# Kernel optimization log

Hardware: AMD Instinct MI355X
Metric: run time of the kernel (lower is better)

The kernel has to match this reference:

```python
import jax, jax.numpy as jnp
import numpy as np

B, N, M, C = 8, 262144, 100, 7
BOX_WEIGHT = 2.0
EPS = 1e-7


def setup_inputs() -> dict:
    key = jax.random.key(0)
    k0, k1, k2, k3, k4, k5 = jax.random.split(key, 6)
    pred_cls = jax.random.normal(k0, (B, N, C), jnp.float32)
    pred_reg = jax.random.normal(k1, (B, N, 4), jnp.float32)
    anchors = jax.random.uniform(k2, (N, 2), jnp.float32) * 1024.0
    strides = jnp.ones((N,), jnp.float32) * 8.0
    ctr = jax.random.uniform(k3, (B, M, 2), jnp.float32) * 960.0 + 32.0
    wh = jax.random.uniform(k4, (B, M, 2), jnp.float32) * 120.0 + 8.0
    gt_boxes = jnp.concatenate([ctr - wh / 2, ctr + wh / 2], axis=-1)
    gt_labels = jax.random.randint(k5, (B, M), 1, C + 1)  # labels in [1, C]
    return {"pred_cls": pred_cls, "pred_reg": pred_reg, "anchors": anchors,
            "strides": strides, "gt_boxes": gt_boxes, "gt_labels": gt_labels}


def giou_loss(p, g):
    # p, g: (M,4) xyxy; elementwise GIoU loss = 1 - GIoU (torchvision semantics)
    ap = (p[:, 2] - p[:, 0]) * (p[:, 3] - p[:, 1])
    ag = (g[:, 2] - g[:, 0]) * (g[:, 3] - g[:, 1])
    lt = jnp.maximum(p[:, :2], g[:, :2])
    rb = jnp.minimum(p[:, 2:], g[:, 2:])
    whi = jnp.clip(rb - lt, 0.0)
    inter = whi[:, 0] * whi[:, 1]
    union = ap + ag - inter
    iou = inter / (union + EPS)
    ltc = jnp.minimum(p[:, :2], g[:, :2])
    rbc = jnp.maximum(p[:, 2:], g[:, 2:])
    whc = jnp.clip(rbc - ltc, 0.0)
    ac = whc[:, 0] * whc[:, 1]
    giou = iou - (ac - union) / (ac + EPS)
    return 1.0 - giou


def reference(pred_cls, pred_reg, anchors, strides, gt_boxes, gt_labels):
    num_anchors = anchors.shape[0]
    # head.decode_boxes: center+offset, exp size decode (guaranteed valid xyxy)
    s = strides[None, :, None]
    ctr = anchors[None] + pred_reg[..., :2] * s
    wh = jnp.exp(pred_reg[..., 2:]) * s
    pred_boxes = jnp.concatenate([ctr - wh / 2, ctr + wh / 2], axis=-1)  # (B,N,4)

    def per_image(cls_b, boxes_b, gt_b, lab_b):
        # nearest-anchor assignment via cdist (expanded as gemm to avoid (M,N,2))
        gc = (gt_b[:, :2] + gt_b[:, 2:]) / 2.0  # (M,2)
        d2 = (jnp.sum(gc * gc, -1)[:, None] + jnp.sum(anchors * anchors, -1)[None, :]
              - 2.0 * gc @ anchors.T)
        dist = jnp.sqrt(jnp.clip(d2, 0.0))  # (M,N)
        assigned = jnp.argmin(dist, axis=1)  # (M,)
        pos_mask = jnp.zeros((num_anchors,), bool).at[assigned].set(True)
        neg_mask = jnp.min(dist, axis=0) > 3.0
        # scatter one-hot class targets (collisions all set 1.0, order-free)
        cls_id = jnp.clip(lab_b - 1, 0, C - 1)
        tgt = jnp.zeros_like(cls_b).at[assigned, cls_id].set(1.0)
        # BCEWithLogits(mean) then scalar * sample_weight then .mean()  (faithful)
        bce_mean = jnp.mean(jnp.logaddexp(0.0, cls_b) - cls_b * tgt)
        sw = jnp.where(pos_mask, 2.0, 1.0) * jnp.where(neg_mask, 1.0, 0.1)
        loss_cls = bce_mean * jnp.mean(sw)
        # box loss: if #unique assigned anchors == M, original pairs boolean-masked
        # (anchor-index-sorted) preds with gt order; else gathers by assigned_idx
        lb_eq = jnp.mean(giou_loss(boxes_b[jnp.sort(assigned)], gt_b))
        lb_ne = jnp.mean(giou_loss(boxes_b[assigned], gt_b))
        loss_box = jnp.where(jnp.sum(pos_mask) == gt_b.shape[0], lb_eq, lb_ne)
        return loss_cls, loss_box

    lc, lb = jax.vmap(per_image)(pred_cls, pred_boxes, gt_boxes, gt_labels)
    total_cls = jnp.mean(lc)
    total_box = jnp.mean(lb)
    return total_cls + BOX_WEIGHT * total_box
```

## Files before the change

### kernel.cpp

```cpp
#include <hip/hip_runtime.h>

#define B_ 8
#define N_ 262144
#define M_ 100
#define C_ 7
#define EPSF 1e-7f
#define AB_ 2048
#define CH_ (N_ / AB_)
#define APT_ 8
#define SEG_ 4
#define SEGN_ (N_ / SEG_)

typedef unsigned long long ull;

__device__ __forceinline__ float softplus0(float x) {
  return fmaxf(x, 0.0f) + log1pf(expf(-fabsf(x)));
}

__device__ __forceinline__ ull u64min(ull a, ull b) { return b < a ? b : a; }

__global__ void __launch_bounds__(256)
k_main(const float* __restrict__ pred_cls,
       const float* __restrict__ anchors,
       const float* __restrict__ gt_boxes,
       double* __restrict__ sp_sum,
       double* __restrict__ swb_sum,
       ull* __restrict__ part) {
  const int b = blockIdx.y;
  const int c = blockIdx.x;
  const int t = threadIdx.x;

  __shared__ float4 gt4[M_];
  __shared__ float red[256];
  __shared__ ull wb[M_][4];

  if (t < M_) {
    float4 g = reinterpret_cast<const float4*>(gt_boxes)[b * M_ + t];
    float gx = __fmul_rn(__fadd_rn(g.x, g.z), 0.5f);
    float gy = __fmul_rn(__fadd_rn(g.y, g.w), 0.5f);
    gt4[t] = make_float4(gx, gy, __fadd_rn(__fmul_rn(gx, gx), __fmul_rn(gy, gy)), 0.f);
  }

  const float4* pc = reinterpret_cast<const float4*>(
      pred_cls + (size_t)b * (size_t)(N_ * C_) + (size_t)c * (AB_ * C_));
  float acc_sp = 0.f;
  for (int k = 0; k < 14; ++k) {
    float4 v = pc[t + k * 256];
    acc_sp += softplus0(v.x) + softplus0(v.y) + softplus0(v.z) + softplus0(v.w);
  }
  red[t] = acc_sp;
  __syncthreads();
  for (int s = 128; s > 0; s >>= 1) {
    if (t < s) red[t] += red[t + s];
    __syncthreads();
  }
  if (t == 0) atomicAdd(&sp_sum[b], (double)red[0]);

  const int n0 = c * AB_;
  float ax[APT_], ay[APT_], t2[APT_], mind[APT_];
  unsigned nn[APT_];
#pragma unroll
  for (int k = 0; k < APT_; ++k) {
    float2 a = reinterpret_cast<const float2*>(anchors)[n0 + t + k * 256];
    ax[k] = a.x; ay[k] = a.y;
    t2[k] = __fadd_rn(__fmul_rn(a.x, a.x), __fmul_rn(a.y, a.y));
    mind[k] = __int_as_float(0x7f800000);
    nn[k] = (unsigned)(n0 + t + (k << 8));
  }
  const int wid  = t >> 6;
  const int lane = t & 63;
  int bidx[6];
#pragma unroll
  for (int i = 0; i < 6; ++i) bidx[i] = ((lane ^ (1 << i)) << 2);
  __syncthreads();

#pragma unroll 2
  for (int m = 0; m < M_; ++m) {
    const float4 g = gt4[m];
    ull pk = 0xffffffffffffffffULL;
#pragma unroll
    for (int k = 0; k < APT_; ++k) {
      float dot = __fmaf_rn(g.y, ay[k], __fmul_rn(g.x, ax[k]));
      float d2  = __fsub_rn(__fadd_rn(g.z, t2[k]), __fadd_rn(dot, dot));
      d2 = fmaxf(d2, 0.0f);
      mind[k] = fminf(mind[k], d2);
      ull cand = ((ull)__float_as_uint(d2) << 32) | (ull)nn[k];
      pk = u64min(pk, cand);
    }
#pragma unroll
    for (int i = 0; i < 6; ++i) {
      int lo = __builtin_amdgcn_ds_bpermute(bidx[i], (int)(unsigned)(pk & 0xffffffffULL));
      int hi = __builtin_amdgcn_ds_bpermute(bidx[i], (int)(unsigned)(pk >> 32));
      ull o = ((ull)(unsigned)hi << 32) | (ull)(unsigned)lo;
      pk = u64min(pk, o);
    }
    if (lane == 0) wb[m][wid] = pk;
  }
  __syncthreads();

  float accw = 0.f;
#pragma unroll
  for (int k = 0; k < APT_; ++k) accw += (sqrtf(mind[k]) > 3.0f) ? 1.0f : 0.1f;
  red[t] = accw;
  __syncthreads();
  for (int s = 128; s > 0; s >>= 1) {
    if (t < s) red[t] += red[t + s];
    __syncthreads();
  }
  if (t == 0) atomicAdd(&swb_sum[b], (double)red[0]);

  if (t < M_) {
    ull v = u64min(u64min(wb[t][0], wb[t][1]), u64min(wb[t][2], wb[t][3]));
    part[((size_t)(b * M_ + t)) * CH_ + c] = v;
  }
}

__global__ void __launch_bounds__(128)
k_final2(const float* __restrict__ pred_cls,
         const float* __restrict__ pred_reg,
         const float* __restrict__ anchors,
         const float* __restrict__ strides,
         const float* __restrict__ gt_boxes,
         const int* __restrict__ gt_labels,
         const ull* __restrict__ part,
         const double* __restrict__ sp_sum,
         const double* __restrict__ swb_sum,
         float* __restrict__ lc, float* __restrict__ lb) {
  const int b = blockIdx.x;
  const int t = threadIdx.x;
  __shared__ unsigned asg[M_];
  __shared__ int cid[M_];
  __shared__ unsigned srt[M_];
  __shared__ float4 gt4[M_];
  __shared__ float red[128];
  __shared__ int dupCount;
  if (t == 0) dupCount = 0;
  if (t < M_) {
    const ull* p = part + ((size_t)(b * M_ + t)) * CH_;
    ull v0 = 0xffffffffffffffffULL, v1 = v0, v2 = v0, v3 = v0;
    for (int c = 0; c < CH_; c += 4) {
      v0 = u64min(v0, p[c]);
      v1 = u64min(v1, p[c + 1]);
      v2 = u64min(v2, p[c + 2]);
      v3 = u64min(v3, p[c + 3]);
    }
    asg[t] = (unsigned)(u64min(u64min(v0, v1), u64min(v2, v3)) & 0xffffffffULL);
    int cc = gt_labels[b * M_ + t] - 1;
    cc = cc < 0 ? 0 : (cc > C_ - 1 ? C_ - 1 : cc);
    cid[t] = cc;
    float4 g = reinterpret_cast<const float4*>(gt_boxes)[b * M_ + t];
    float gx = __fmul_rn(__fadd_rn(g.x, g.z), 0.5f);
    float gy = __fmul_rn(__fadd_rn(g.y, g.w), 0.5f);
    gt4[t] = make_float4(gx, gy, __fadd_rn(__fmul_rn(gx, gx), __fmul_rn(gy, gy)), 0.f);
  }
  __syncthreads();

  float tg = 0.f, corr = 0.f;
  if (t < M_) {
    bool dupPair = false, dupIdx = false;
    for (int m = 0; m < t; ++m) {
      if (asg[m] == asg[t]) {
        dupIdx = true;
        if (cid[m] == cid[t]) dupPair = true;
      }
    }
    if (!dupPair) tg = pred_cls[((size_t)b * N_ + asg[t]) * C_ + cid[t]];
    if (dupIdx) atomicAdd(&dupCount, 1);
    if (!dupIdx) {
      float2 a = reinterpret_cast<const float2*>(anchors)[asg[t]];
      float t2 = __fadd_rn(__fmul_rn(a.x, a.x), __fmul_rn(a.y, a.y));
      float mind = __int_as_float(0x7f800000);
      for (int m = 0; m < M_; ++m) {
        float4 g = gt4[m];
        float dot = __fmaf_rn(g.y, a.y, __fmul_rn(g.x, a.x));
        float d2  = __fsub_rn(__fadd_rn(g.z, t2), __fadd_rn(dot, dot));
        mind = fminf(mind, fmaxf(d2, 0.0f));
      }
      corr = (sqrtf(mind) > 3.0f) ? 1.0f : 0.1f;
    }
  }
  red[t] = tg;
  __syncthreads();
  for (int s = 64; s > 0; s >>= 1) {
    if (t < s) red[t] += red[t + s];
    __syncthreads();
  }
  const float tgt_total = red[0];
  __syncthreads();
  red[t] = corr;
  __syncthreads();
  for (int s = 64; s > 0; s >>= 1) {
    if (t < s) red[t] += red[t + s];
    __syncthreads();
  }
  const float corr_total = red[0];
  const bool uniqueAll = (dupCount == 0);
  __syncthreads();

  if (uniqueAll && t < M_) {
    const unsigned v = asg[t];
    int rank = 0;
    for (int m = 0; m < M_; ++m) rank += (asg[m] < v) ? 1 : 0;
    srt[rank] = v;
  }
  __syncthreads();

  float gl = 0.f;
  if (t < M_) {
    const unsigned q = uniqueAll ? srt[t] : asg[t];
    float4 r = reinterpret_cast<const float4*>(pred_reg)[(size_t)b * N_ + q];
    float2 a = reinterpret_cast<const float2*>(anchors)[q];
    float s = strides[q];
    float cx = a.x + r.x * s, cy = a.y + r.y * s;
    float hx = (expf(r.z) * s) * 0.5f, hy = (expf(r.w) * s) * 0.5f;
    float px0 = cx - hx, py0 = cy - hy, px1 = cx + hx, py1 = cy + hy;
    float4 g = reinterpret_cast<const float4*>(gt_boxes)[b * M_ + t];
    float ap = (px1 - px0) * (py1 - py0);
    float ag = (g.z - g.x) * (g.w - g.y);
    float ltx = fmaxf(px0, g.x), lty = fmaxf(py0, g.y);
    float rbx = fminf(px1, g.z), rby = fminf(py1, g.w);
    float wix = fmaxf(rbx - ltx, 0.f), wiy = fmaxf(rby - lty, 0.f);
    float inter = wix * wiy;
    float uni = ap + ag - inter;
    float iou = inter / (uni + EPSF);
    float lcx = fminf(px0, g.x), lcy = fminf(py0, g.y);
    float rcx = fmaxf(px1, g.z), rcy = fmaxf(py1, g.w);
    float wcx = fmaxf(rcx - lcx, 0.f), wcy = fmaxf(rcy - lcy, 0.f);
    float ac = wcx * wcy;
    float giou = iou - (ac - uni) / (ac + EPSF);
    gl = 1.f - giou;
  }
  __syncthreads();
  red[t] = gl;
  __syncthreads();
  for (int s = 64; s > 0; s >>= 1) {
    if (t < s) red[t] += red[t + s];
    __syncthreads();
  }
  if (t == 0) {
    lb[b] = red[0] / (float)M_;
    float bce = (float)((sp_sum[b] - (double)tgt_total) / (double)(N_ * C_));
    float swm = (float)((swb_sum[b] + (double)corr_total) / (double)N_);
    lc[b] = bce * swm;
  }
}

__global__ void __launch_bounds__(256)
k_passA(const float* __restrict__ pred_cls,
        const float* __restrict__ anchors,
        const float* __restrict__ gt_boxes,
        double* __restrict__ sp_sum,
        double* __restrict__ swb_sum) {
  const int b = blockIdx.y;
  const int c = blockIdx.x;
  const int t = threadIdx.x;
  __shared__ float4 gt4[M_];
  __shared__ float red[256];
  if (t < M_) {
    float4 g = reinterpret_cast<const float4*>(gt_boxes)[b * M_ + t];
    float gx = __fmul_rn(__fadd_rn(g.x, g.z), 0.5f);
    float gy = __fmul_rn(__fadd_rn(g.y, g.w), 0.5f);
    gt4[t] = make_float4(gx, gy, __fadd_rn(__fmul_rn(gx, gx), __fmul_rn(gy, gy)), 0.f);
  }
  const float4* pc = reinterpret_cast<const float4*>(
      pred_cls + (size_t)b * (size_t)(N_ * C_) + (size_t)c * (1024 * C_));
  float acc_sp = 0.f;
#pragma unroll
  for (int k = 0; k < 7; ++k) {
    float4 v = pc[t + k * 256];
    acc_sp += softplus0(v.x) + softplus0(v.y) + softplus0(v.z) + softplus0(v.w);
  }
  red[t] = acc_sp;
  __syncthreads();
  for (int s = 128; s > 0; s >>= 1) {
    if (t < s) red[t] += red[t + s];
    __syncthreads();
  }
  if (t == 0) atomicAdd(&sp_sum[b], (double)red[0]);
  const int n0 = c * 1024;
  float ax[4], ay[4], t2[4], mind[4];
#pragma unroll
  for (int k = 0; k < 4; ++k) {
    float2 a = reinterpret_cast<const float2*>(anchors)[n0 + t + k * 256];
    ax[k] = a.x; ay[k] = a.y;
    t2[k] = __fadd_rn(__fmul_rn(a.x, a.x), __fmul_rn(a.y, a.y));
    mind[k] = __int_as_float(0x7f800000);
  }
#pragma unroll 2
  for (int m = 0; m < M_; ++m) {
    const float4 g = gt4[m];
#pragma unroll
    for (int k = 0; k < 4; ++k) {
      float dot = __fmaf_rn(g.y, ay[k], __fmul_rn(g.x, ax[k]));
      float d2  = __fsub_rn(__fadd_rn(g.z, t2[k]), __fadd_rn(dot, dot));
      mind[k] = fminf(mind[k], fmaxf(d2, 0.0f));
    }
  }
  float accw = 0.f;
#pragma unroll
  for (int k = 0; k < 4; ++k) accw += (sqrtf(mind[k]) > 3.0f) ? 1.0f : 0.1f;
  __syncthreads();
  red[t] = accw;
  __syncthreads();
  for (int s = 128; s > 0; s >>= 1) {
    if (t < s) red[t] += red[t + s];
    __syncthreads();
  }
  if (t == 0) atomicAdd(&swb_sum[b], (double)red[0]);
}

__global__ void __launch_bounds__(256)
k_argmin(const float* __restrict__ anchors,
         const float* __restrict__ gt_boxes,
         ull* __restrict__ amin) {
  const int bm  = blockIdx.y;
  const int seg = blockIdx.x;
  const float4 g = reinterpret_cast<const float4*>(gt_boxes)[bm];
  const float gx = __fmul_rn(__fadd_rn(g.x, g.z), 0.5f);
  const float gy = __fmul_rn(__fadd_rn(g.y, g.w), 0.5f);
  const float t1 = __fadd_rn(__fmul_rn(gx, gx), __fmul_rn(gy, gy));
  const float2* an = reinterpret_cast<const float2*>(anchors);
  float best = __int_as_float(0x7f800000);
  unsigned bestn = 0;
  const int n0 = seg * SEGN_;
#pragma unroll 4
  for (int n = n0 + threadIdx.x; n < n0 + SEGN_; n += 256) {
    float2 a = an[n];
    float t2  = __fadd_rn(__fmul_rn(a.x, a.x), __fmul_rn(a.y, a.y));
    float dot = __fmaf_rn(gy, a.y, __fmul_rn(gx, a.x));
    float d2  = __fsub_rn(__fadd_rn(t1, t2), __fadd_rn(dot, dot));
    d2 = fmaxf(d2, 0.0f);
    if (d2 < best) { best = d2; bestn = (unsigned)n; }
  }
  ull pk = ((ull)__float_as_uint(best) << 32) | (ull)bestn;
  __shared__ ull red[256];
  const int t = threadIdx.x;
  red[t] = pk;
  __syncthreads();
  for (int s = 128; s > 0; s >>= 1) {
    if (t < s) {
      ull o = red[t + s];
      if (o < red[t]) red[t] = o;
    }
    __syncthreads();
  }
  if (t == 0) atomicMin(&amin[bm], red[0]);
}

__global__ void __launch_bounds__(128)
k_final_img(const float* __restrict__ pred_cls,
            const float* __restrict__ pred_reg,
            const float* __restrict__ anchors,
            const float* __restrict__ strides,
            const float* __restrict__ gt_boxes,
            const int* __restrict__ gt_labels,
            const ull* __restrict__ amin,
            const double* __restrict__ sp_sum,
            const double* __restrict__ swb_sum,
            float* __restrict__ lc, float* __restrict__ lb) {
  const int b = blockIdx.x;
  const int t = threadIdx.x;
  __shared__ unsigned asg[M_];
  __shared__ int cid[M_];
  __shared__ unsigned srt[M_];
  __shared__ float4 gt4[M_];
  __shared__ float red[128];
  __shared__ int dupCount;
  if (t == 0) dupCount = 0;
  if (t < M_) {
    asg[t] = (unsigned)(amin[b * M_ + t] & 0xffffffffULL);
    int c = gt_labels[b * M_ + t] - 1;
    c = c < 0 ? 0 : (c > C_ - 1 ? C_ - 1 : c);
    cid[t] = c;
    float4 g = reinterpret_cast<const float4*>(gt_boxes)[b * M_ + t];
    float gx = __fmul_rn(__fadd_rn(g.x, g.z), 0.5f);
    float gy = __fmul_rn(__fadd_rn(g.y, g.w), 0.5f);
    gt4[t] = make_float4(gx, gy, __fadd_rn(__fmul_rn(gx, gx), __fmul_rn(gy, gy)), 0.f);
  }
  __syncthreads();

  float tg = 0.f, corr = 0.f;
  if (t < M_) {
    bool dupPair = false, dupIdx = false;
    for (int m = 0; m < t; ++m) {
      if (asg[m] == asg[t]) {
        dupIdx = true;
        if (cid[m] == cid[t]) dupPair = true;
      }
    }
    if (!dupPair) tg = pred_cls[((size_t)b * N_ + asg[t]) * C_ + cid[t]];
    if (dupIdx) atomicAdd(&dupCount, 1);
    if (!dupIdx) {
      float2 a = reinterpret_cast<const float2*>(anchors)[asg[t]];
      float t2 = __fadd_rn(__fmul_rn(a.x, a.x), __fmul_rn(a.y, a.y));
      float mind = __int_as_float(0x7f800000);
      for (int m = 0; m < M_; ++m) {
        float4 g = gt4[m];
        float dot = __fmaf_rn(g.y, a.y, __fmul_rn(g.x, a.x));
        float d2  = __fsub_rn(__fadd_rn(g.z, t2), __fadd_rn(dot, dot));
        mind = fminf(mind, fmaxf(d2, 0.0f));
      }
      corr = (sqrtf(mind) > 3.0f) ? 1.0f : 0.1f;
    }
  }
  red[t] = tg;
  __syncthreads();
  for (int s = 64; s > 0; s >>= 1) {
    if (t < s) red[t] += red[t + s];
    __syncthreads();
  }
  const float tgt_total = red[0];
  __syncthreads();
  red[t] = corr;
  __syncthreads();
  for (int s = 64; s > 0; s >>= 1) {
    if (t < s) red[t] += red[t + s];
    __syncthreads();
  }
  const float corr_total = red[0];
  const bool uniqueAll = (dupCount == 0);
  __syncthreads();

  if (uniqueAll && t < M_) {
    const unsigned v = asg[t];
    int rank = 0;
    for (int m = 0; m < M_; ++m) rank += (asg[m] < v) ? 1 : 0;
    srt[rank] = v;
  }
  __syncthreads();

  float gl = 0.f;
  if (t < M_) {
    const unsigned q = uniqueAll ? srt[t] : asg[t];
    float4 r = reinterpret_cast<const float4*>(pred_reg)[(size_t)b * N_ + q];
    float2 a = reinterpret_cast<const float2*>(anchors)[q];
    float s = strides[q];
    float cx = a.x + r.x * s, cy = a.y + r.y * s;
    float hx = (expf(r.z) * s) * 0.5f, hy = (expf(r.w) * s) * 0.5f;
    float px0 = cx - hx, py0 = cy - hy, px1 = cx + hx, py1 = cy + hy;
    float4 g = reinterpret_cast<const float4*>(gt_boxes)[b * M_ + t];
    float ap = (px1 - px0) * (py1 - py0);
    float ag = (g.z - g.x) * (g.w - g.y);
    float ltx = fmaxf(px0, g.x), lty = fmaxf(py0, g.y);
    float rbx = fminf(px1, g.z), rby = fminf(py1, g.w);
    float wix = fmaxf(rbx - ltx, 0.f), wiy = fmaxf(rby - lty, 0.f);
    float inter = wix * wiy;
    float uni = ap + ag - inter;
    float iou = inter / (uni + EPSF);
    float lcx = fminf(px0, g.x), lcy = fminf(py0, g.y);
    float rcx = fmaxf(px1, g.z), rcy = fmaxf(py1, g.w);
    float wcx = fmaxf(rcx - lcx, 0.f), wcy = fmaxf(rcy - lcy, 0.f);
    float ac = wcx * wcy;
    float giou = iou - (ac - uni) / (ac + EPSF);
    gl = 1.f - giou;
  }
  __syncthreads();
  red[t] = gl;
  __syncthreads();
  for (int s = 64; s > 0; s >>= 1) {
    if (t < s) red[t] += red[t + s];
    __syncthreads();
  }
  if (t == 0) {
    lb[b] = red[0] / (float)M_;
    float bce = (float)((sp_sum[b] - (double)tgt_total) / (double)(N_ * C_));
    float swm = (float)((swb_sum[b] + (double)corr_total) / (double)N_);
    lc[b] = bce * swm;
  }
}

__global__ void __launch_bounds__(64)
k_total(const float* __restrict__ lc, const float* __restrict__ lb,
        float* __restrict__ out) {
  if (threadIdx.x == 0 && blockIdx.x == 0) {
    float sc = 0.f, sb = 0.f;
    for (int b = 0; b < B_; ++b) { sc += lc[b]; sb += lb[b]; }
    out[0] = sc / 8.0f + 2.0f * (sb / 8.0f);
  }
}

extern "C" void kernel_launch(void* const* d_in, const int* in_sizes, int n_in,
                              void* d_out, int out_size, void* d_ws, size_t ws_size,
                              hipStream_t stream) {
  (void)in_sizes; (void)n_in; (void)out_size;
  const float* pred_cls  = (const float*)d_in[0];
  const float* pred_reg  = (const float*)d_in[1];
  const float* anchors   = (const float*)d_in[2];
  const float* strides   = (const float*)d_in[3];
  const float* gt_boxes  = (const float*)d_in[4];
  const int*   gt_labels = (const int*)d_in[5];
  float* out = (float*)d_out;

  char* ws = (char*)d_ws;
  double* sp_sum  = (double*)(ws);
  double* swb_sum = (double*)(ws + 64);

  const size_t part_off = 128;
  const size_t part_bytes = (size_t)B_ * M_ * CH_ * 8;
  const size_t tail_off = part_off + part_bytes;
  const size_t need = tail_off + 64 + 64;

  if (ws_size >= need) {
    ull* part = (ull*)(ws + part_off);
    float* lc = (float*)(ws + tail_off);
    float* lb = (float*)(ws + tail_off + 64);

    hipMemsetAsync(ws, 0, 128, stream);
    k_main<<<dim3(CH_, B_), dim3(256), 0, stream>>>(pred_cls, anchors, gt_boxes,
                                                    sp_sum, swb_sum, part);
    k_final2<<<dim3(B_), dim3(128), 0, stream>>>(pred_cls, pred_reg, anchors,
                                                 strides, gt_boxes, gt_labels,
                                                 part, sp_sum, swb_sum, lc, lb);
    k_total<<<dim3(1), dim3(64), 0, stream>>>(lc, lb, out);
  } else {
    ull* amin = (ull*)(ws + 128);
    float* lc = (float*)(ws + 128 + 6400);
    float* lb = (float*)(ws + 128 + 6400 + 32);
    hipMemsetAsync(ws, 0, 128, stream);
    hipMemsetAsync(ws + 128, 0xFF, 6400, stream);
    k_passA<<<dim3(N_ / 1024, B_), dim3(256), 0, stream>>>(pred_cls, anchors, gt_boxes,
                                                           sp_sum, swb_sum);
    k_argmin<<<dim3(SEG_, B_ * M_), dim3(256), 0, stream>>>(anchors, gt_boxes, amin);
    k_final_img<<<dim3(B_), dim3(128), 0, stream>>>(pred_cls, pred_reg, anchors,
                                                    strides, gt_boxes, gt_labels,
                                                    amin, sp_sum, swb_sum, lc, lb);
    k_total<<<dim3(1), dim3(64), 0, stream>>>(lc, lb, out);
  }
}
```

Baseline: 249.5 us.

## Pack distance math, shorten shuffle tree, fuse final kernels into one launch

Anchor distance computation now uses 2-wide float vectors so packed FMA/min/max can be used. Each thread first picks its best local anchor with scalar compares and only a 3-step cross-lane shuffle runs per gt box, with the remaining reduction done through shared memory. Double atomics are replaced by per-block partial sums, which drops the memset. The per-image final kernel and the total kernel are merged into a single 1024-thread block. The aims are less ALU and shuffle work in the hot loop and fewer launches, at the cost of a larger shared-memory reduction and a serial tail in one block.

Result: slower. 261.0 us (+4.6%).

```diff
diff --git a/kernel.cpp b/kernel.cpp
--- a/kernel.cpp
+++ b/kernel.cpp
@@ -7,11 +7,11 @@
 #define EPSF 1e-7f
 #define AB_ 2048
 #define CH_ (N_ / AB_)
-#define APT_ 8
 #define SEG_ 4
 #define SEGN_ (N_ / SEG_)
 
 typedef unsigned long long ull;
+typedef float v2f __attribute__((ext_vector_type(2)));
 
 __device__ __forceinline__ float softplus0(float x) {
   return fmaxf(x, 0.0f) + log1pf(expf(-fabsf(x)));
@@ -23,8 +23,8 @@
 k_main(const float* __restrict__ pred_cls,
        const float* __restrict__ anchors,
        const float* __restrict__ gt_boxes,
-       double* __restrict__ sp_sum,
-       double* __restrict__ swb_sum,
+       float* __restrict__ sp_part,
+       float* __restrict__ sw_part,
        ull* __restrict__ part) {
   const int b = blockIdx.y;
   const int c = blockIdx.x;
@@ -32,7 +32,7 @@
 
   __shared__ float4 gt4[M_];
   __shared__ float red[256];
-  __shared__ ull wb[M_][4];
+  __shared__ ull wb[M_][33];
 
   if (t < M_) {
     float4 g = reinterpret_cast<const float4*>(gt_boxes)[b * M_ + t];
@@ -54,124 +54,164 @@
     if (t < s) red[t] += red[t + s];
     __syncthreads();
   }
-  if (t == 0) atomicAdd(&sp_sum[b], (double)red[0]);
+  if (t == 0) sp_part[b * CH_ + c] = red[0];
 
   const int n0 = c * AB_;
-  float ax[APT_], ay[APT_], t2[APT_], mind[APT_];
-  unsigned nn[APT_];
-#pragma unroll
-  for (int k = 0; k < APT_; ++k) {
-    float2 a = reinterpret_cast<const float2*>(anchors)[n0 + t + k * 256];
-    ax[k] = a.x; ay[k] = a.y;
-    t2[k] = __fadd_rn(__fmul_rn(a.x, a.x), __fmul_rn(a.y, a.y));
-    mind[k] = __int_as_float(0x7f800000);
-    nn[k] = (unsigned)(n0 + t + (k << 8));
-  }
-  const int wid  = t >> 6;
+  const float2* an = reinterpret_cast<const float2*>(anchors);
+  v2f ax2[4], ay2[4], t22[4], mind2[4];
+#pragma unroll
+  for (int q = 0; q < 4; ++q) {
+    float2 a0 = an[n0 + t + (2 * q) * 256];
+    float2 a1 = an[n0 + t + (2 * q + 1) * 256];
+    ax2[q] = (v2f){a0.x, a1.x};
+    ay2[q] = (v2f){a0.y, a1.y};
+    t22[q] = (v2f){__fadd_rn(__fmul_rn(a0.x, a0.x), __fmul_rn(a0.y, a0.y)),
+                   __fadd_rn(__fmul_rn(a1.x, a1.x), __fmul_rn(a1.y, a1.y))};
+    mind2[q] = (v2f){__int_as_float(0x7f800000), __int_as_float(0x7f800000)};
+  }
   const int lane = t & 63;
-  int bidx[6];
-#pragma unroll
-  for (int i = 0; i < 6; ++i) bidx[i] = ((lane ^ (1 << i)) << 2);
-  __syncthreads();
-
+  int bidx[3];
+#pragma unroll
+  for (int i = 0; i < 3; ++i) bidx[i] = ((lane ^ (1 << i)) << 2);
+  __syncthreads();
+
+  const v2f zero2 = (v2f){0.f, 0.f};
 #pragma unroll 2
   for (int m = 0; m < M_; ++m) {
     const float4 g = gt4[m];
-    ull pk = 0xffffffffffffffffULL;
-#pragma unroll
-    for (int k = 0; k < APT_; ++k) {
-      float dot = __fmaf_rn(g.y, ay[k], __fmul_rn(g.x, ax[k]));
-      float d2  = __fsub_rn(__fadd_rn(g.z, t2[k]), __fadd_rn(dot, dot));
-      d2 = fmaxf(d2, 0.0f);
-      mind[k] = fminf(mind[k], d2);
-      ull cand = ((ull)__float_as_uint(d2) << 32) | (ull)nn[k];
-      pk = u64min(pk, cand);
-    }
-#pragma unroll
-    for (int i = 0; i < 6; ++i) {
+    const v2f gx2 = (v2f){g.x, g.x};
+    const v2f gy2 = (v2f){g.y, g.y};
+    const v2f gz2 = (v2f){g.z, g.z};
+    float bd = __int_as_float(0x7f800000);
+    int bk = 0;
+#pragma unroll
+    for (int q = 0; q < 4; ++q) {
+      v2f gmul = gx2 * ax2[q];
+      v2f dot  = __builtin_elementwise_fma(gy2, ay2[q], gmul);
+      v2f d2   = (gz2 + t22[q]) - (dot + dot);
+      d2 = __builtin_elementwise_max(d2, zero2);
+      mind2[q] = __builtin_elementwise_min(mind2[q], d2);
+      if (d2.x < bd) { bd = d2.x; bk = 2 * q; }
+      if (d2.y < bd) { bd = d2.y; bk = 2 * q + 1; }
+    }
+    ull pk = ((ull)__float_as_uint(bd) << 32) |
+             (ull)(unsigned)(n0 + t + (bk << 8));
+#pragma unroll
+    for (int i = 0; i < 3; ++i) {
       int lo = __builtin_amdgcn_ds_bpermute(bidx[i], (int)(unsigned)(pk & 0xffffffffULL));
       int hi = __builtin_amdgcn_ds_bpermute(bidx[i], (int)(unsigned)(pk >> 32));
       ull o = ((ull)(unsigned)hi << 32) | (ull)(unsigned)lo;
       pk = u64min(pk, o);
     }
-    if (lane == 0) wb[m][wid] = pk;
+    if ((t & 7) == 0) wb[m][t >> 3] = pk;
   }
   __syncthreads();
 
   float accw = 0.f;
 #pragma unroll
-  for (int k = 0; k < APT_; ++k) accw += (sqrtf(mind[k]) > 3.0f) ? 1.0f : 0.1f;
+  for (int q = 0; q < 4; ++q) {
+    accw += (sqrtf(mind2[q].x) > 3.0f) ? 1.0f : 0.1f;
+    accw += (sqrtf(mind2[q].y) > 3.0f) ? 1.0f : 0.1f;
+  }
   red[t] = accw;
   __syncthreads();
   for (int s = 128; s > 0; s >>= 1) {
     if (t < s) red[t] += red[t + s];
     __syncthreads();
   }
-  if (t == 0) atomicAdd(&swb_sum[b], (double)red[0]);
+  if (t == 0) sw_part[b * CH_ + c] = red[0];
 
   if (t < M_) {
-    ull v = u64min(u64min(wb[t][0], wb[t][1]), u64min(wb[t][2], wb[t][3]));
-    part[((size_t)(b * M_ + t)) * CH_ + c] = v;
-  }
-}
-
-__global__ void __launch_bounds__(128)
-k_final2(const float* __restrict__ pred_cls,
-         const float* __restrict__ pred_reg,
-         const float* __restrict__ anchors,
-         const float* __restrict__ strides,
-         const float* __restrict__ gt_boxes,
-         const int* __restrict__ gt_labels,
-         const ull* __restrict__ part,
-         const double* __restrict__ sp_sum,
-         const double* __restrict__ swb_sum,
-         float* __restrict__ lc, float* __restrict__ lb) {
-  const int b = blockIdx.x;
-  const int t = threadIdx.x;
-  __shared__ unsigned asg[M_];
-  __shared__ int cid[M_];
-  __shared__ unsigned srt[M_];
-  __shared__ float4 gt4[M_];
-  __shared__ float red[128];
-  __shared__ int dupCount;
-  if (t == 0) dupCount = 0;
-  if (t < M_) {
-    const ull* p = part + ((size_t)(b * M_ + t)) * CH_;
-    ull v0 = 0xffffffffffffffffULL, v1 = v0, v2 = v0, v3 = v0;
-    for (int c = 0; c < CH_; c += 4) {
+    const ull* w = wb[t];
+    ull v0 = w[0], v1 = w[1], v2 = w[2], v3 = w[3];
+    for (int j = 4; j < 32; j += 4) {
+      v0 = u64min(v0, w[j]);
+      v1 = u64min(v1, w[j + 1]);
+      v2 = u64min(v2, w[j + 2]);
+      v3 = u64min(v3, w[j + 3]);
+    }
+    part[((size_t)(b * M_ + t)) * CH_ + c] = u64min(u64min(v0, v1), u64min(v2, v3));
+  }
+}
+
+__global__ void __launch_bounds__(1024)
+k_finalall(const float* __restrict__ pred_cls,
+           const float* __restrict__ pred_reg,
+           const float* __restrict__ anchors,
+           const float* __restrict__ strides,
+           const float* __restrict__ gt_boxes,
+           const int* __restrict__ gt_labels,
+           const ull* __restrict__ part,
+           const float* __restrict__ sp_part,
+           const float* __restrict__ sw_part,
+           float* __restrict__ out) {
+  const int t  = threadIdx.x;
+  const int b  = t >> 7;
+  const int tt = t & 127;
+  __shared__ float4 gt4[B_][M_];
+  __shared__ unsigned asg[B_][M_];
+  __shared__ int cid[B_][M_];
+  __shared__ unsigned srt[B_][M_];
+  __shared__ float red[B_][128];
+  __shared__ double redd[B_][128];
+  __shared__ int dup[B_];
+  __shared__ float tgtT[B_], corrT[B_], lcs[B_], lbs[B_];
+  __shared__ double spT[B_], swT[B_];
+
+  if (tt == 0) dup[b] = 0;
+  if (tt < M_) {
+    const ull* p = part + ((size_t)(b * M_ + tt)) * CH_;
+    ull v0 = p[0], v1 = p[1], v2 = p[2], v3 = p[3];
+    for (int c = 4; c < CH_; c += 4) {
       v0 = u64min(v0, p[c]);
       v1 = u64min(v1, p[c + 1]);
       v2 = u64min(v2, p[c + 2]);
       v3 = u64min(v3, p[c + 3]);
     }
-    asg[t] = (unsigned)(u64min(u64min(v0, v1), u64min(v2, v3)) & 0xffffffffULL);
-    int cc = gt_labels[b * M_ + t] - 1;
+    asg[b][tt] = (unsigned)(u64min(u64min(v0, v1), u64min(v2, v3)) & 0xffffffffULL);
+    int cc = gt_labels[b * M_ + tt] - 1;
     cc = cc < 0 ? 0 : (cc > C_ - 1 ? C_ - 1 : cc);
-    cid[t] = cc;
-    float4 g = reinterpret_cast<const float4*>(gt_boxes)[b * M_ + t];
+    cid[b][tt] = cc;
+    float4 g = reinterpret_cast<const float4*>(gt_boxes)[b * M_ + tt];
     float gx = __fmul_rn(__fadd_rn(g.x, g.z), 0.5f);
     float gy = __fmul_rn(__fadd_rn(g.y, g.w), 0.5f);
-    gt4[t] = make_float4(gx, gy, __fadd_rn(__fmul_rn(gx, gx), __fmul_rn(gy, gy)), 0.f);
-  }
+    gt4[b][tt] = make_float4(gx, gy, __fadd_rn(__fmul_rn(gx, gx), __fmul_rn(gy, gy)), 0.f);
+  }
+
+  redd[b][tt] = (double)sp_part[b * CH_ + tt];
+  __syncthreads();
+  for (int s = 64; s > 0; s >>= 1) {
+    if (tt < s) redd[b][tt] += redd[b][tt + s];
+    __syncthreads();
+  }
+  if (tt == 0) spT[b] = redd[b][0];
+  __syncthreads();
+  redd[b][tt] = (double)sw_part[b * CH_ + tt];
+  __syncthreads();
+  for (int s = 64; s > 0; s >>= 1) {
+    if (tt < s) redd[b][tt] += redd[b][tt + s];
+    __syncthreads();
+  }
+  if (tt == 0) swT[b] = redd[b][0];
   __syncthreads();
 
   float tg = 0.f, corr = 0.f;
-  if (t < M_) {
+  if (tt < M_) {
     bool dupPair = false, dupIdx = false;
-    for (int m = 0; m < t; ++m) {
-      if (asg[m] == asg[t]) {
+    for (int m = 0; m < tt; ++m) {
+      if (asg[b][m] == asg[b][tt]) {
         dupIdx = true;
-        if (cid[m] == cid[t]) dupPair = true;
+        if (cid[b][m] == cid[b][tt]) dupPair = true;
       }
     }
-    if (!dupPair) tg = pred_cls[((size_t)b * N_ + asg[t]) * C_ + cid[t]];
-    if (dupIdx) atomicAdd(&dupCount, 1);
+    if (!dupPair) tg = pred_cls[((size_t)b * N_ + asg[b][tt]) * C_ + cid[b][tt]];
+    if (dupIdx) atomicAdd(&dup[b], 1);
     if (!dupIdx) {
-      float2 a = reinterpret_cast<const float2*>(anchors)[asg[t]];
+      float2 a = reinterpret_cast<const float2*>(anchors)[asg[b][tt]];
       float t2 = __fadd_rn(__fmul_rn(a.x, a.x), __fmul_rn(a.y, a.y));
       float mind = __int_as_float(0x7f800000);
       for (int m = 0; m < M_; ++m) {
-        float4 g = gt4[m];
+        float4 g = gt4[b][m];
         float dot = __fmaf_rn(g.y, a.y, __fmul_rn(g.x, a.x));
         float d2  = __fsub_rn(__fadd_rn(g.z, t2), __fadd_rn(dot, dot));
         mind = fminf(mind, fmaxf(d2, 0.0f));
@@ -179,42 +219,42 @@
       corr = (sqrtf(mind) > 3.0f) ? 1.0f : 0.1f;
     }
   }
-  red[t] = tg;
-  __syncthreads();
-  for (int s = 64; s > 0; s >>= 1) {
-    if (t < s) red[t] += red[t + s];
-    __syncthreads();
-  }
-  const float tgt_total = red[0];
-  __syncthreads();
-  red[t] = corr;
-  __syncthreads();
-  for (int s = 64; s > 0; s >>= 1) {
-    if (t < s) red[t] += red[t + s];
-    __syncthreads();
-  }
-  const float corr_total = red[0];
-  const bool uniqueAll = (dupCount == 0);
-  __syncthreads();
-
-  if (uniqueAll && t < M_) {
-    const unsigned v = asg[t];
+  red[b][tt] = tg;
+  __syncthreads();
+  for (int s = 64; s > 0; s >>= 1) {
+    if (tt < s) red[b][tt] += red[b][tt + s];
+    __syncthreads();
+  }
+  if (tt == 0) tgtT[b] = red[b][0];
+  __syncthreads();
+  red[b][tt] = corr;
+  __syncthreads();
+  for (int s = 64; s > 0; s >>= 1) {
+    if (tt < s) red[b][tt] += red[b][tt + s];
+    __syncthreads();
+  }
+  if (tt == 0) corrT[b] = red[b][0];
+  __syncthreads();
+  const bool uniqueAll = (dup[b] == 0);
+
+  if (uniqueAll && tt < M_) {
+    const unsigned v = asg[b][tt];
     int rank = 0;
-    for (int m = 0; m < M_; ++m) rank += (asg[m] < v) ? 1 : 0;
-    srt[rank] = v;
+    for (int m = 0; m < M_; ++m) rank += (asg[b][m] < v) ? 1 : 0;
+    srt[b][rank] = v;
   }
   __syncthreads();
 
   float gl = 0.f;
-  if (t < M_) {
-    const unsigned q = uniqueAll ? srt[t] : asg[t];
+  if (tt < M_) {
+    const unsigned q = uniqueAll ? srt[b][tt] : asg[b][tt];
     float4 r = reinterpret_cast<const float4*>(pred_reg)[(size_t)b * N_ + q];
     float2 a = reinterpret_cast<const float2*>(anchors)[q];
     float s = strides[q];
     float cx = a.x + r.x * s, cy = a.y + r.y * s;
     float hx = (expf(r.z) * s) * 0.5f, hy = (expf(r.w) * s) * 0.5f;
     float px0 = cx - hx, py0 = cy - hy, px1 = cx + hx, py1 = cy + hy;
-    float4 g = reinterpret_cast<const float4*>(gt_boxes)[b * M_ + t];
+    float4 g = reinterpret_cast<const float4*>(gt_boxes)[b * M_ + tt];
     float ap = (px1 - px0) * (py1 - py0);
     float ag = (g.z - g.x) * (g.w - g.y);
     float ltx = fmaxf(px0, g.x), lty = fmaxf(py0, g.y);
@@ -231,17 +271,23 @@
     gl = 1.f - giou;
   }
   __syncthreads();
-  red[t] = gl;
-  __syncthreads();
-  for (int s = 64; s > 0; s >>= 1) {
-    if (t < s) red[t] += red[t + s];
-    __syncthreads();
-  }
+  red[b][tt] = gl;
+  __syncthreads();
+  for (int s = 64; s > 0; s >>= 1) {
+    if (tt < s) red[b][tt] += red[b][tt + s];
+    __syncthreads();
+  }
+  if (tt == 0) {
+    lbs[b] = red[b][0] / (float)M_;
+    float bce = (float)((spT[b] - (double)tgtT[b]) / (double)(N_ * C_));
+    float swm = (float)((swT[b] + (double)corrT[b]) / (double)N_);
+    lcs[b] = bce * swm;
+  }
+  __syncthreads();
   if (t == 0) {
-    lb[b] = red[0] / (float)M_;
-    float bce = (float)((sp_sum[b] - (double)tgt_total) / (double)(N_ * C_));
-    float swm = (float)((swb_sum[b] + (double)corr_total) / (double)N_);
-    lc[b] = bce * swm;
+    float sc = 0.f, sb = 0.f;
+    for (int i = 0; i < B_; ++i) { sc += lcs[i]; sb += lbs[i]; }
+    out[0] = sc / 8.0f + 2.0f * (sb / 8.0f);
   }
 }
 
@@ -492,27 +538,23 @@
   float* out = (float*)d_out;
 
   char* ws = (char*)d_ws;
-  double* sp_sum  = (double*)(ws);
-  double* swb_sum = (double*)(ws + 64);
-
-  const size_t part_off = 128;
   const size_t part_bytes = (size_t)B_ * M_ * CH_ * 8;
-  const size_t tail_off = part_off + part_bytes;
-  const size_t need = tail_off + 64 + 64;
+  const size_t sp_off = part_bytes;
+  const size_t sw_off = sp_off + 4096;
+  const size_t need   = sw_off + 4096;
 
   if (ws_size >= need) {
-    ull* part = (ull*)(ws + part_off);
-    float* lc = (float*)(ws + tail_off);
-    float* lb = (float*)(ws + tail_off + 64);
-
-    hipMemsetAsync(ws, 0, 128, stream);
+    ull*   part    = (ull*)ws;
+    float* sp_part = (float*)(ws + sp_off);
+    float* sw_part = (float*)(ws + sw_off);
     k_main<<<dim3(CH_, B_), dim3(256), 0, stream>>>(pred_cls, anchors, gt_boxes,
-                                                    sp_sum, swb_sum, part);
-    k_final2<<<dim3(B_), dim3(128), 0, stream>>>(pred_cls, pred_reg, anchors,
-                                                 strides, gt_boxes, gt_labels,
-                                                 part, sp_sum, swb_sum, lc, lb);
-    k_total<<<dim3(1), dim3(64), 0, stream>>>(lc, lb, out);
+                                                    sp_part, sw_part, part);
+    k_finalall<<<dim3(1), dim3(1024), 0, stream>>>(pred_cls, pred_reg, anchors,
+                                                   strides, gt_boxes, gt_labels,
+                                                   part, sp_part, sw_part, out);
   } else {
+    double* sp_sum  = (double*)(ws);
+    double* swb_sum = (double*)(ws + 64);
     ull* amin = (ull*)(ws + 128);
     float* lc = (float*)(ws + 128 + 6400);
     float* lb = (float*)(ws + 128 + 6400 + 32);
```

## Replace brute-force anchor distance scan with uniform-grid spatial hashing

Applied to the files above, without the earlier changes.

Builds a 64x64 uniform grid over the anchors (count, scan, scatter) and uses it to find each GT's nearest anchor through expanding ring search. The same grid marks anchors within radius 3 of any GT in a byte map, which replaces the full M×N min-distance pass. This removes the O(B·M·N) distance computation that dominated k_main. In exchange it adds several small kernels, scattered gathers through the grid and a memset of a B·N byte map, and it relies on the ring termination bound being conservative enough to give exact ties.

Result: faster. 225.6 us (-9.6%).

```diff
diff --git a/kernel.cpp b/kernel.cpp
--- a/kernel.cpp
+++ b/kernel.cpp
@@ -7,11 +7,15 @@
 #define EPSF 1e-7f
 #define AB_ 2048
 #define CH_ (N_ / AB_)
-#define APT_ 8
+#define GXC 64
+#define CELLW 16.0f
+#define INV_CELL 0.0625f
+#define NCELL (GXC * GXC)
 #define SEG_ 4
 #define SEGN_ (N_ / SEG_)
 
 typedef unsigned long long ull;
+typedef unsigned int u32;
 
 __device__ __forceinline__ float softplus0(float x) {
   return fmaxf(x, 0.0f) + log1pf(expf(-fabsf(x)));
@@ -19,28 +23,135 @@
 
 __device__ __forceinline__ ull u64min(ull a, ull b) { return b < a ? b : a; }
 
+__device__ __forceinline__ int cell_of(float2 a) {
+  int ix = (int)(a.x * INV_CELL); ix = ix < 0 ? 0 : (ix > GXC - 1 ? GXC - 1 : ix);
+  int iy = (int)(a.y * INV_CELL); iy = iy < 0 ? 0 : (iy > GXC - 1 ? GXC - 1 : iy);
+  return iy * GXC + ix;
+}
+
+__device__ __forceinline__ float d2_exact(float gx, float gy, float t1, float2 a) {
+  float t2  = __fadd_rn(__fmul_rn(a.x, a.x), __fmul_rn(a.y, a.y));
+  float dot = __fmaf_rn(gy, a.y, __fmul_rn(gx, a.x));
+  return __fsub_rn(__fadd_rn(t1, t2), __fadd_rn(dot, dot));
+}
+
 __global__ void __launch_bounds__(256)
-k_main(const float* __restrict__ pred_cls,
-       const float* __restrict__ anchors,
-       const float* __restrict__ gt_boxes,
-       double* __restrict__ sp_sum,
-       double* __restrict__ swb_sum,
-       ull* __restrict__ part) {
-  const int b = blockIdx.y;
-  const int c = blockIdx.x;
+k_count(const float* __restrict__ anchors, u32* __restrict__ hist) {
+  const int n = blockIdx.x * 256 + threadIdx.x;
+  float2 a = reinterpret_cast<const float2*>(anchors)[n];
+  atomicAdd(&hist[cell_of(a)], 1u);
+}
+
+__global__ void __launch_bounds__(1024)
+k_scan(u32* __restrict__ hist ,
+       u32* __restrict__ cellStart) {
+  __shared__ u32 sA[1024];
   const int t = threadIdx.x;
-
-  __shared__ float4 gt4[M_];
+  u32 h0 = hist[4 * t], h1 = hist[4 * t + 1], h2 = hist[4 * t + 2], h3 = hist[4 * t + 3];
+  u32 s = h0 + h1 + h2 + h3;
+  sA[t] = s;
+  __syncthreads();
+  for (int off = 1; off < 1024; off <<= 1) {
+    u32 add = (t >= off) ? sA[t - off] : 0u;
+    __syncthreads();
+    sA[t] += add;
+    __syncthreads();
+  }
+  u32 excl = sA[t] - s;
+  u32 e0 = excl, e1 = e0 + h0, e2 = e1 + h1, e3 = e2 + h2;
+  cellStart[4 * t] = e0; cellStart[4 * t + 1] = e1;
+  cellStart[4 * t + 2] = e2; cellStart[4 * t + 3] = e3;
+  hist[4 * t] = e0; hist[4 * t + 1] = e1;
+  hist[4 * t + 2] = e2; hist[4 * t + 3] = e3;
+  if (t == 1023) cellStart[NCELL] = sA[1023];
+}
+
+__global__ void __launch_bounds__(256)
+k_scatter(const float* __restrict__ anchors, u32* __restrict__ cur,
+          u32* __restrict__ aidx) {
+  const int n = blockIdx.x * 256 + threadIdx.x;
+  float2 a = reinterpret_cast<const float2*>(anchors)[n];
+  u32 pos = atomicAdd(&cur[cell_of(a)], 1u);
+  aidx[pos] = (u32)n;
+}
+
+__global__ void __launch_bounds__(64)
+k_assign(const float* __restrict__ anchors,
+         const float* __restrict__ gt_boxes,
+         const u32* __restrict__ cellStart,
+         const u32* __restrict__ aidx,
+         unsigned char* __restrict__ map,
+         ull* __restrict__ amin) {
+  const int m = blockIdx.x, b = blockIdx.y;
+  const int lane = threadIdx.x;
+  const float4 g = reinterpret_cast<const float4*>(gt_boxes)[b * M_ + m];
+  const float gx = __fmul_rn(__fadd_rn(g.x, g.z), 0.5f);
+  const float gy = __fmul_rn(__fadd_rn(g.y, g.w), 0.5f);
+  const float t1 = __fadd_rn(__fmul_rn(gx, gx), __fmul_rn(gy, gy));
+  const float2* an = reinterpret_cast<const float2*>(anchors);
+  unsigned char* mp = map + (size_t)b * N_;
+
+  {
+    int x0 = (int)floorf((gx - 3.5f) * INV_CELL); x0 = x0 < 0 ? 0 : (x0 > GXC - 1 ? GXC - 1 : x0);
+    int x1 = (int)floorf((gx + 3.5f) * INV_CELL); x1 = x1 < 0 ? 0 : (x1 > GXC - 1 ? GXC - 1 : x1);
+    int y0 = (int)floorf((gy - 3.5f) * INV_CELL); y0 = y0 < 0 ? 0 : (y0 > GXC - 1 ? GXC - 1 : y0);
+    int y1 = (int)floorf((gy + 3.5f) * INV_CELL); y1 = y1 < 0 ? 0 : (y1 > GXC - 1 ? GXC - 1 : y1);
+    for (int cy = y0; cy <= y1; ++cy)
+      for (int cx = x0; cx <= x1; ++cx) {
+        u32 s = cellStart[cy * GXC + cx], e = cellStart[cy * GXC + cx + 1];
+        for (u32 j = s + lane; j < e; j += 64) {
+          u32 n = aidx[j];
+          if (d2_exact(gx, gy, t1, an[n]) <= 9.0f) mp[n] = 1;
+        }
+      }
+  }
+
+  int cx0 = (int)(gx * INV_CELL); cx0 = cx0 < 0 ? 0 : (cx0 > GXC - 1 ? GXC - 1 : cx0);
+  int cy0 = (int)(gy * INV_CELL); cy0 = cy0 < 0 ? 0 : (cy0 > GXC - 1 ? GXC - 1 : cy0);
+  int bidx[6];
+#pragma unroll
+  for (int i = 0; i < 6; ++i) bidx[i] = ((lane ^ (1 << i)) << 2);
+
+  ull best = 0xffffffffffffffffULL;
+  for (int ring = 1; ring < GXC; ++ring) {
+    best = 0xffffffffffffffffULL;
+    int x0 = cx0 - ring < 0 ? 0 : cx0 - ring;
+    int x1 = cx0 + ring > GXC - 1 ? GXC - 1 : cx0 + ring;
+    int y0 = cy0 - ring < 0 ? 0 : cy0 - ring;
+    int y1 = cy0 + ring > GXC - 1 ? GXC - 1 : cy0 + ring;
+    for (int cy = y0; cy <= y1; ++cy)
+      for (int cx = x0; cx <= x1; ++cx) {
+        u32 s = cellStart[cy * GXC + cx], e = cellStart[cy * GXC + cx + 1];
+        for (u32 j = s + lane; j < e; j += 64) {
+          u32 n = aidx[j];
+          float d2c = fmaxf(d2_exact(gx, gy, t1, an[n]), 0.0f);
+          best = u64min(best, ((ull)__float_as_uint(d2c) << 32) | (ull)n);
+        }
+      }
+#pragma unroll
+    for (int i = 0; i < 6; ++i) {
+      int lo = __builtin_amdgcn_ds_bpermute(bidx[i], (int)(u32)(best & 0xffffffffULL));
+      int hi = __builtin_amdgcn_ds_bpermute(bidx[i], (int)(u32)(best >> 32));
+      best = u64min(best, ((ull)(u32)hi << 32) | (ull)(u32)lo);
+    }
+    float lx = (cx0 - ring < 0)       ? 1e18f : gx - CELLW * (float)(cx0 - ring);
+    float hx = (cx0 + ring > GXC - 1) ? 1e18f : CELLW * (float)(cx0 + ring + 1) - gx;
+    float ly = (cy0 - ring < 0)       ? 1e18f : gy - CELLW * (float)(cy0 - ring);
+    float hy = (cy0 + ring > GXC - 1) ? 1e18f : CELLW * (float)(cy0 + ring + 1) - gy;
+    float cov = fminf(fminf(lx, hx), fminf(ly, hy));
+    float bf = __uint_as_float((u32)(best >> 32));
+    if (bf <= cov * cov - 4.0f) break;
+  }
+  if (lane == 0) amin[b * M_ + m] = best;
+}
+
+__global__ void __launch_bounds__(256)
+k_sp_sw(const float* __restrict__ pred_cls,
+        const unsigned char* __restrict__ map,
+        float* __restrict__ sp_part,
+        float* __restrict__ sw_part) {
+  const int b = blockIdx.y, c = blockIdx.x, t = threadIdx.x;
   __shared__ float red[256];
-  __shared__ ull wb[M_][4];
-
-  if (t < M_) {
-    float4 g = reinterpret_cast<const float4*>(gt_boxes)[b * M_ + t];
-    float gx = __fmul_rn(__fadd_rn(g.x, g.z), 0.5f);
-    float gy = __fmul_rn(__fadd_rn(g.y, g.w), 0.5f);
-    gt4[t] = make_float4(gx, gy, __fadd_rn(__fmul_rn(gx, gx), __fmul_rn(gy, gy)), 0.f);
-  }
-
   const float4* pc = reinterpret_cast<const float4*>(
       pred_cls + (size_t)b * (size_t)(N_ * C_) + (size_t)c * (AB_ * C_));
   float acc_sp = 0.f;
@@ -54,105 +165,65 @@
     if (t < s) red[t] += red[t + s];
     __syncthreads();
   }
-  if (t == 0) atomicAdd(&sp_sum[b], (double)red[0]);
-
-  const int n0 = c * AB_;
-  float ax[APT_], ay[APT_], t2[APT_], mind[APT_];
-  unsigned nn[APT_];
-#pragma unroll
-  for (int k = 0; k < APT_; ++k) {
-    float2 a = reinterpret_cast<const float2*>(anchors)[n0 + t + k * 256];
-    ax[k] = a.x; ay[k] = a.y;
-    t2[k] = __fadd_rn(__fmul_rn(a.x, a.x), __fmul_rn(a.y, a.y));
-    mind[k] = __int_as_float(0x7f800000);
-    nn[k] = (unsigned)(n0 + t + (k << 8));
-  }
-  const int wid  = t >> 6;
-  const int lane = t & 63;
-  int bidx[6];
-#pragma unroll
-  for (int i = 0; i < 6; ++i) bidx[i] = ((lane ^ (1 << i)) << 2);
-  __syncthreads();
-
-#pragma unroll 2
-  for (int m = 0; m < M_; ++m) {
-    const float4 g = gt4[m];
-    ull pk = 0xffffffffffffffffULL;
-#pragma unroll
-    for (int k = 0; k < APT_; ++k) {
-      float dot = __fmaf_rn(g.y, ay[k], __fmul_rn(g.x, ax[k]));
-      float d2  = __fsub_rn(__fadd_rn(g.z, t2[k]), __fadd_rn(dot, dot));
-      d2 = fmaxf(d2, 0.0f);
-      mind[k] = fminf(mind[k], d2);
-      ull cand = ((ull)__float_as_uint(d2) << 32) | (ull)nn[k];
-      pk = u64min(pk, cand);
-    }
-#pragma unroll
-    for (int i = 0; i < 6; ++i) {
-      int lo = __builtin_amdgcn_ds_bpermute(bidx[i], (int)(unsigned)(pk & 0xffffffffULL));
-      int hi = __builtin_amdgcn_ds_bpermute(bidx[i], (int)(unsigned)(pk >> 32));
-      ull o = ((ull)(unsigned)hi << 32) | (ull)(unsigned)lo;
-      pk = u64min(pk, o);
-    }
-    if (lane == 0) wb[m][wid] = pk;
-  }
-  __syncthreads();
-
+  if (t == 0) sp_part[b * CH_ + c] = red[0];
+
+  const unsigned char* mp = map + (size_t)b * N_ + (size_t)c * AB_;
   float accw = 0.f;
 #pragma unroll
-  for (int k = 0; k < APT_; ++k) accw += (sqrtf(mind[k]) > 3.0f) ? 1.0f : 0.1f;
+  for (int k = 0; k < 8; ++k) accw += mp[t + k * 256] ? 0.1f : 1.0f;
+  __syncthreads();
   red[t] = accw;
   __syncthreads();
   for (int s = 128; s > 0; s >>= 1) {
     if (t < s) red[t] += red[t + s];
     __syncthreads();
   }
-  if (t == 0) atomicAdd(&swb_sum[b], (double)red[0]);
-
-  if (t < M_) {
-    ull v = u64min(u64min(wb[t][0], wb[t][1]), u64min(wb[t][2], wb[t][3]));
-    part[((size_t)(b * M_ + t)) * CH_ + c] = v;
-  }
+  if (t == 0) sw_part[b * CH_ + c] = red[0];
 }
 
 __global__ void __launch_bounds__(128)
-k_final2(const float* __restrict__ pred_cls,
+k_final3(const float* __restrict__ pred_cls,
          const float* __restrict__ pred_reg,
          const float* __restrict__ anchors,
          const float* __restrict__ strides,
          const float* __restrict__ gt_boxes,
          const int* __restrict__ gt_labels,
-         const ull* __restrict__ part,
-         const double* __restrict__ sp_sum,
-         const double* __restrict__ swb_sum,
+         const ull* __restrict__ amin,
+         const unsigned char* __restrict__ map,
+         const float* __restrict__ sp_part,
+         const float* __restrict__ sw_part,
          float* __restrict__ lc, float* __restrict__ lb) {
   const int b = blockIdx.x;
   const int t = threadIdx.x;
   __shared__ unsigned asg[M_];
   __shared__ int cid[M_];
   __shared__ unsigned srt[M_];
-  __shared__ float4 gt4[M_];
   __shared__ float red[128];
+  __shared__ double redd[128];
   __shared__ int dupCount;
+  __shared__ double spT, swT;
   if (t == 0) dupCount = 0;
   if (t < M_) {
-    const ull* p = part + ((size_t)(b * M_ + t)) * CH_;
-    ull v0 = 0xffffffffffffffffULL, v1 = v0, v2 = v0, v3 = v0;
-    for (int c = 0; c < CH_; c += 4) {
-      v0 = u64min(v0, p[c]);
-      v1 = u64min(v1, p[c + 1]);
-      v2 = u64min(v2, p[c + 2]);
-      v3 = u64min(v3, p[c + 3]);
-    }
-    asg[t] = (unsigned)(u64min(u64min(v0, v1), u64min(v2, v3)) & 0xffffffffULL);
+    asg[t] = (unsigned)(amin[b * M_ + t] & 0xffffffffULL);
     int cc = gt_labels[b * M_ + t] - 1;
     cc = cc < 0 ? 0 : (cc > C_ - 1 ? C_ - 1 : cc);
     cid[t] = cc;
-    float4 g = reinterpret_cast<const float4*>(gt_boxes)[b * M_ + t];
-    float gx = __fmul_rn(__fadd_rn(g.x, g.z), 0.5f);
-    float gy = __fmul_rn(__fadd_rn(g.y, g.w), 0.5f);
-    gt4[t] = make_float4(gx, gy, __fadd_rn(__fmul_rn(gx, gx), __fmul_rn(gy, gy)), 0.f);
-  }
+  }
+  redd[t] = (double)sp_part[b * CH_ + t];
+  __syncthreads();
+  for (int s = 64; s > 0; s >>= 1) {
+    if (t < s) redd[t] += redd[t + s];
+    __syncthreads();
+  }
+  if (t == 0) spT = redd[0];
+  __syncthreads();
+  redd[t] = (double)sw_part[b * CH_ + t];
+  __syncthreads();
+  for (int s = 64; s > 0; s >>= 1) {
+    if (t < s) redd[t] += redd[t + s];
+    __syncthreads();
+  }
+  if (t == 0) swT = redd[0];
   __syncthreads();
 
   float tg = 0.f, corr = 0.f;
@@ -166,18 +237,7 @@
     }
     if (!dupPair) tg = pred_cls[((size_t)b * N_ + asg[t]) * C_ + cid[t]];
     if (dupIdx) atomicAdd(&dupCount, 1);
-    if (!dupIdx) {
-      float2 a = reinterpret_cast<const float2*>(anchors)[asg[t]];
-      float t2 = __fadd_rn(__fmul_rn(a.x, a.x), __fmul_rn(a.y, a.y));
-      float mind = __int_as_float(0x7f800000);
-      for (int m = 0; m < M_; ++m) {
-        float4 g = gt4[m];
-        float dot = __fmaf_rn(g.y, a.y, __fmul_rn(g.x, a.x));
-        float d2  = __fsub_rn(__fadd_rn(g.z, t2), __fadd_rn(dot, dot));
-        mind = fminf(mind, fmaxf(d2, 0.0f));
-      }
-      corr = (sqrtf(mind) > 3.0f) ? 1.0f : 0.1f;
-    }
+    if (!dupIdx) corr = map[(size_t)b * N_ + asg[t]] ? 0.1f : 1.0f;
   }
   red[t] = tg;
   __syncthreads();
@@ -239,9 +299,19 @@
   }
   if (t == 0) {
     lb[b] = red[0] / (float)M_;
-    float bce = (float)((sp_sum[b] - (double)tgt_total) / (double)(N_ * C_));
-    float swm = (float)((swb_sum[b] + (double)corr_total) / (double)N_);
+    float bce = (float)((spT - (double)tgt_total) / (double)(N_ * C_));
+    float swm = (float)((swT + (double)corr_total) / (double)N_);
     lc[b] = bce * swm;
+  }
+}
+
+__global__ void __launch_bounds__(64)
+k_total(const float* __restrict__ lc, const float* __restrict__ lb,
+        float* __restrict__ out) {
+  if (threadIdx.x == 0 && blockIdx.x == 0) {
+    float sc = 0.f, sb = 0.f;
+    for (int b = 0; b < B_; ++b) { sc += lc[b]; sb += lb[b]; }
+    out[0] = sc / 8.0f + 2.0f * (sb / 8.0f);
   }
 }
 
@@ -326,9 +396,7 @@
 #pragma unroll 4
   for (int n = n0 + threadIdx.x; n < n0 + SEGN_; n += 256) {
     float2 a = an[n];
-    float t2  = __fadd_rn(__fmul_rn(a.x, a.x), __fmul_rn(a.y, a.y));
-    float dot = __fmaf_rn(gy, a.y, __fmul_rn(gx, a.x));
-    float d2  = __fsub_rn(__fadd_rn(t1, t2), __fadd_rn(dot, dot));
+    float d2 = d2_exact(gx, gy, t1, a);
     d2 = fmaxf(d2, 0.0f);
     if (d2 < best) { best = d2; bestn = (unsigned)n; }
   }
@@ -378,7 +446,6 @@
     gt4[t] = make_float4(gx, gy, __fadd_rn(__fmul_rn(gx, gx), __fmul_rn(gy, gy)), 0.f);
   }
   __syncthreads();
-
   float tg = 0.f, corr = 0.f;
   if (t < M_) {
     bool dupPair = false, dupIdx = false;
@@ -420,7 +487,6 @@
   const float corr_total = red[0];
   const bool uniqueAll = (dupCount == 0);
   __syncthreads();
-
   if (uniqueAll && t < M_) {
     const unsigned v = asg[t];
     int rank = 0;
@@ -428,7 +494,6 @@
     srt[rank] = v;
   }
   __syncthreads();
-
   float gl = 0.f;
   if (t < M_) {
     const unsigned q = uniqueAll ? srt[t] : asg[t];
@@ -469,16 +534,6 @@
   }
 }
 
-__global__ void __launch_bounds__(64)
-k_total(const float* __restrict__ lc, const float* __restrict__ lb,
-        float* __restrict__ out) {
-  if (threadIdx.x == 0 && blockIdx.x == 0) {
-    float sc = 0.f, sb = 0.f;
-    for (int b = 0; b < B_; ++b) { sc += lc[b]; sb += lb[b]; }
-    out[0] = sc / 8.0f + 2.0f * (sb / 8.0f);
-  }
-}
-
 extern "C" void kernel_launch(void* const* d_in, const int* in_sizes, int n_in,
                               void* d_out, int out_size, void* d_ws, size_t ws_size,
                               hipStream_t stream) {
@@ -492,27 +547,43 @@
   float* out = (float*)d_out;
 
   char* ws = (char*)d_ws;
-  double* sp_sum  = (double*)(ws);
-  double* swb_sum = (double*)(ws + 64);
-
-  const size_t part_off = 128;
-  const size_t part_bytes = (size_t)B_ * M_ * CH_ * 8;
-  const size_t tail_off = part_off + part_bytes;
-  const size_t need = tail_off + 64 + 64;
+  const size_t off_cs   = 0;
+  const size_t off_cur  = 16512;
+  const size_t off_aidx = off_cur + 16384;
+  const size_t off_map  = off_aidx + 1048576;
+  const size_t off_sp   = off_map + (size_t)B_ * N_;
+  const size_t off_sw   = off_sp + 4096;
+  const size_t off_amin = off_sw + 4096;
+  const size_t off_lc   = off_amin + 6400;
+  const size_t off_lb   = off_lc + 64;
+  const size_t need     = off_lb + 64;
 
   if (ws_size >= need) {
-    ull* part = (ull*)(ws + part_off);
-    float* lc = (float*)(ws + tail_off);
-    float* lb = (float*)(ws + tail_off + 64);
-
-    hipMemsetAsync(ws, 0, 128, stream);
-    k_main<<<dim3(CH_, B_), dim3(256), 0, stream>>>(pred_cls, anchors, gt_boxes,
-                                                    sp_sum, swb_sum, part);
-    k_final2<<<dim3(B_), dim3(128), 0, stream>>>(pred_cls, pred_reg, anchors,
-                                                 strides, gt_boxes, gt_labels,
-                                                 part, sp_sum, swb_sum, lc, lb);
+    u32* cellStart = (u32*)(ws + off_cs);
+    u32* cur       = (u32*)(ws + off_cur);
+    u32* aidx      = (u32*)(ws + off_aidx);
+    unsigned char* map = (unsigned char*)(ws + off_map);
+    float* sp_part = (float*)(ws + off_sp);
+    float* sw_part = (float*)(ws + off_sw);
+    ull*   amin    = (ull*)(ws + off_amin);
+    float* lc      = (float*)(ws + off_lc);
+    float* lb      = (float*)(ws + off_lb);
+
+    hipMemsetAsync(cur, 0, 16384, stream);
+    hipMemsetAsync(map, 0, (size_t)B_ * N_, stream);
+    k_count<<<dim3(N_ / 256), dim3(256), 0, stream>>>(anchors, cur);
+    k_scan<<<dim3(1), dim3(1024), 0, stream>>>(cur, cellStart);
+    k_scatter<<<dim3(N_ / 256), dim3(256), 0, stream>>>(anchors, cur, aidx);
+    k_assign<<<dim3(M_, B_), dim3(64), 0, stream>>>(anchors, gt_boxes, cellStart,
+                                                    aidx, map, amin);
+    k_sp_sw<<<dim3(CH_, B_), dim3(256), 0, stream>>>(pred_cls, map, sp_part, sw_part);
+    k_final3<<<dim3(B_), dim3(128), 0, stream>>>(pred_cls, pred_reg, anchors, strides,
+                                                 gt_boxes, gt_labels, amin, map,
+                                                 sp_part, sw_part, lc, lb);
     k_total<<<dim3(1), dim3(64), 0, stream>>>(lc, lb, out);
   } else {
+    double* sp_sum  = (double*)(ws);
+    double* swb_sum = (double*)(ws + 64);
     ull* amin = (ull*)(ws + 128);
     float* lc = (float*)(ws + 128 + 6400);
     float* lb = (float*)(ws + 128 + 6400 + 32);
```
